# Kernel optimization log

Hardware: AMD Instinct MI355X
Metric: run time of the kernel (lower is better)

## Reference

```python
import jax, jax.numpy as jnp
import numpy as np
from jax.scipy.special import logsumexp

B, L, DIN, H, NL, E = 32, 1024, 2048, 1024, 21, 768
LN_EPS = 1e-5

def setup_inputs() -> dict:
    key = jax.random.key(0)
    ks = jax.random.split(key, 8)
    return {
        "seq_feats": jax.random.normal(ks[0], (B, L, DIN), jnp.float32),
        "labels": jax.random.randint(ks[1], (B, L), 0, NL),
        "attention_mask": jnp.ones((B, L), jnp.bool_),
        "W_tok": jax.random.normal(ks[2], (DIN, H), jnp.float32) * 0.02,
        "ln_gamma": jnp.ones((H,), jnp.float32),
        "ln_beta": jnp.zeros((H,), jnp.float32),
        "label_table": jax.random.normal(ks[3], (NL, E), jnp.float32) * 0.02,
        "W_lab": jax.random.normal(ks[4], (E, H), jnp.float32) * 0.02,
        "temperature": jnp.float32(10.0),
        "start_trans": jax.random.uniform(ks[5], (NL,), jnp.float32, -0.1, 0.1),
        "end_trans": jax.random.uniform(ks[6], (NL,), jnp.float32, -0.1, 0.1),
        "trans": jax.random.uniform(ks[7], (NL, NL), jnp.float32, -0.1, 0.1),
    }

def _crf_nll(logits, labels, mask, start_trans, end_trans, trans):
    # torchcrf CRF(batch_first=True), reduction='mean': loss = -mean_b llh_b
    mf = mask.astype(logits.dtype)  # (B,L)
    # --- numerator: score of the gold path ---
    emit = jnp.take_along_axis(logits, labels[..., None], axis=-1)[..., 0]  # (B,L)
    score = start_trans[labels[:, 0]] + emit[:, 0]
    score = score + (emit[:, 1:] * mf[:, 1:]).sum(-1)
    score = score + (trans[labels[:, :-1], labels[:, 1:]] * mf[:, 1:]).sum(-1)
    last_idx = mask.sum(-1).astype(jnp.int32) - 1  # (B,)
    last_tag = jnp.take_along_axis(labels, last_idx[:, None], axis=1)[:, 0]
    score = score + end_trans[last_tag]
    # --- denominator: log partition via forward algorithm (lax.scan over time) ---
    alpha0 = start_trans[None, :] + logits[:, 0]  # (B,NL)
    def step(alpha, xs):
        emit_t, m_t = xs  # (B,NL), (B,)
        new = logsumexp(alpha[:, :, None] + trans[None, :, :] + emit_t[:, None, :], axis=1)
        return jnp.where(m_t[:, None], new, alpha), None
    xs = (jnp.moveaxis(logits[:, 1:], 1, 0), jnp.moveaxis(mask[:, 1:], 1, 0))
    alpha, _ = jax.lax.scan(step, alpha0, xs)
    logZ = logsumexp(alpha + end_trans[None, :], axis=-1)  # (B,)
    return -(score - logZ).mean()

def reference(seq_feats, labels, attention_mask, W_tok, ln_gamma, ln_beta,
              label_table, W_lab, temperature, start_trans, end_trans, trans):
    # token_proj: Linear(no bias) -> LayerNorm -> GELU (exact) -> Dropout(eval=no-op)
    h = seq_feats @ W_tok  # (B,L,H)
    mu = h.mean(-1, keepdims=True)
    var = h.var(-1, keepdims=True)
    h = (h - mu) / jnp.sqrt(var + LN_EPS) * ln_gamma + ln_beta
    token_h = jax.nn.gelu(h, approximate=False)
    label_h = label_table @ W_lab  # (NL,H)
    logits = jnp.einsum('blh,nh->bln', token_h, label_h) * temperature
    loss = _crf_nll(logits, labels, attention_mask, start_trans, end_trans, trans)
    return logits, loss
```

## Files before the change

kernel.cpp:

```cpp
#include <hip/hip_runtime.h>
#include <math.h>

typedef __attribute__((ext_vector_type(8))) short bf16x8;
typedef __attribute__((ext_vector_type(4))) float f32x4;
typedef unsigned short u16;

#define Bsz 32
#define Lsz 1024
#define DIN 2048
#define Hsz 1024
#define NLB 21
#define CCH 64
#define TCH 16

__device__ __forceinline__ float b2f(u16 u) {
  union { unsigned int i; float f; } v; v.i = ((unsigned int)u) << 16; return v.f;
}
__device__ __forceinline__ u16 f2b(float f) {
  union { float f; unsigned int i; } v; v.f = f;
  unsigned int r = v.i + 0x7fffu + ((v.i >> 16) & 1u);
  return (u16)(r >> 16);
}

__global__ void k_convA(const float* __restrict__ in, u16* __restrict__ out, int n4) {
  int idx = blockIdx.x * blockDim.x + threadIdx.x;
  int stride = gridDim.x * blockDim.x;
  const float4* in4 = (const float4*)in;
  ushort4* out4 = (ushort4*)out;
  for (int i = idx; i < n4; i += stride) {
    float4 v = in4[i];
    ushort4 o;
    o.x = f2b(v.x); o.y = f2b(v.y); o.z = f2b(v.z); o.w = f2b(v.w);
    out4[i] = o;
  }
}

__global__ void k_convWT(const float* __restrict__ W, u16* __restrict__ Wt) {
  __shared__ float tile[64][65];
  const int ntile = blockIdx.x & 15;
  const int ktile = blockIdx.x >> 4;
  const int n0 = ntile * 64, k0 = ktile * 64;
  const int tid = threadIdx.x;
#pragma unroll
  for (int i = 0; i < 16; ++i) {
    int lin = i * 256 + tid;
    int r = lin >> 6, c = lin & 63;
    tile[r][c] = W[(size_t)(k0 + r) * Hsz + n0 + c];
  }
  __syncthreads();
#pragma unroll
  for (int i = 0; i < 16; ++i) {
    int lin = i * 256 + tid;
    int r = lin >> 6, c = lin & 63;
    Wt[(size_t)(n0 + r) * DIN + k0 + c] = f2b(tile[c][r]);
  }
}

__global__ void k_trW(const float* __restrict__ WL, float* __restrict__ WLt) {
  __shared__ float tile[64][65];
  const int nt = blockIdx.x & 15;
  const int et = blockIdx.x >> 4;
  const int n0 = nt * 64, e0 = et * 64;
  const int tid = threadIdx.x;
#pragma unroll
  for (int i = 0; i < 16; ++i) {
    int lin = i * 256 + tid;
    int r = lin >> 6, c = lin & 63;
    tile[r][c] = WL[(size_t)(e0 + r) * Hsz + n0 + c];
  }
  __syncthreads();
#pragma unroll
  for (int i = 0; i < 16; ++i) {
    int lin = i * 256 + tid;
    int r = lin >> 6, c = lin & 63;
    WLt[(size_t)(n0 + r) * 768 + e0 + c] = tile[c][r];
  }
}

__global__ __launch_bounds__(256) void k_labelh(const float* __restrict__ LT, const float* __restrict__ WLt,
                                                u16* __restrict__ LH) {
  const int tid = threadIdx.x;
  const int lane = tid & 63;
  const int wave = tid >> 6;
  const int wid = blockIdx.x * 4 + wave;
  const int row = wid >> 10;
  const int col = wid & 1023;
  const float4* a4 = (const float4*)(LT + (size_t)row * 768);
  const float4* b4 = (const float4*)(WLt + (size_t)col * 768);
  float p = 0.f;
#pragma unroll
  for (int it = 0; it < 3; ++it) {
    float4 a = a4[it * 64 + lane];
    float4 b = b4[it * 64 + lane];
    p += a.x * b.x + a.y * b.y + a.z * b.z + a.w * b.w;
  }
#pragma unroll
  for (int o = 32; o; o >>= 1) p += __shfl_xor(p, o);
  if (lane == 0) LH[(size_t)row * Hsz + col] = f2b(p);
}

__global__ __launch_bounds__(256) void k_gemm(const u16* __restrict__ A, const u16* __restrict__ Bt,
                                              u16* __restrict__ H) {
  __shared__ u16 sA[128 * 64];
  __shared__ u16 sB[128 * 64];
  const int tid = threadIdx.x;
  const int lane = tid & 63;
  const int wave = tid >> 6;
  const int m0 = (blockIdx.x >> 3) * 128;
  const int n0 = (blockIdx.x & 7) * 128;
  const int wm = (wave >> 1) * 64;
  const int wn = (wave & 1) * 64;

  f32x4 acc[4][4];
#pragma unroll
  for (int i = 0; i < 4; ++i)
#pragma unroll
    for (int j = 0; j < 4; ++j) acc[i][j] = (f32x4){0.f, 0.f, 0.f, 0.f};

  for (int k0 = 0; k0 < DIN; k0 += 64) {
#pragma unroll
    for (int q = 0; q < 4; ++q) {
      int idx = q * 256 + tid;
      int row = idx >> 3;
      int cl = (idx & 7) ^ (row & 7);
      const u16* ga = A + (size_t)(m0 + row) * DIN + k0 + cl * 8;
      __builtin_amdgcn_global_load_lds((const __attribute__((address_space(1))) void*)ga,
                                       (__attribute__((address_space(3))) void*)&sA[idx * 8], 16, 0, 0);
      const u16* gb = Bt + (size_t)(n0 + row) * DIN + k0 + cl * 8;
      __builtin_amdgcn_global_load_lds((const __attribute__((address_space(1))) void*)gb,
                                       (__attribute__((address_space(3))) void*)&sB[idx * 8], 16, 0, 0);
    }
    __syncthreads();
#pragma unroll
    for (int ks = 0; ks < 2; ++ks) {
      bf16x8 af[4], bfr[4];
      const int quad = lane >> 4;
      const int ck = ks * 4 + quad;
#pragma unroll
      for (int t = 0; t < 4; ++t) {
        int m = wm + t * 16 + (lane & 15);
        af[t] = *(const bf16x8*)&sA[m * 64 + ((ck ^ (m & 7)) * 8)];
        int n = wn + t * 16 + (lane & 15);
        bfr[t] = *(const bf16x8*)&sB[n * 64 + ((ck ^ (n & 7)) * 8)];
      }
#pragma unroll
      for (int i = 0; i < 4; ++i)
#pragma unroll
        for (int j = 0; j < 4; ++j)
          acc[i][j] = __builtin_amdgcn_mfma_f32_16x16x32_bf16(af[i], bfr[j], acc[i][j], 0, 0, 0);
    }
    __syncthreads();
  }
#pragma unroll
  for (int i = 0; i < 4; ++i) {
#pragma unroll
    for (int j = 0; j < 4; ++j) {
      int col = n0 + wn + j * 16 + (lane & 15);
      int r0 = m0 + wm + i * 16 + ((lane >> 4) << 2);
#pragma unroll
      for (int r = 0; r < 4; ++r) H[(size_t)(r0 + r) * Hsz + col] = f2b(acc[i][j][r]);
    }
  }
}

__global__ __launch_bounds__(256) void k_head(const u16* __restrict__ Hb, const u16* __restrict__ LH,
                                              const float* __restrict__ gamma, const float* __restrict__ beta,
                                              const float* __restrict__ tempp, float* __restrict__ logits) {
  __shared__ u16 sLH[32 * Hsz];
  const int tid = threadIdx.x;
  const int lane = tid & 63;
  const int wave = tid >> 6;
  for (int id = tid; id < 32 * 64; id += 256) {
    int n = id >> 6, c = id & 63;
    uint4 v = (uint4){0u, 0u, 0u, 0u};
    if (n < NLB) v = *(const uint4*)(LH + (size_t)n * Hsz + c * 8);
    *(uint4*)&sLH[((n << 6) | ((c & 56) | ((c ^ n) & 7))) * 8] = v;
  }
  const float T = tempp[0];
  __syncthreads();

  const int m = lane & 15;
  const int q = lane >> 4;
  const int tok = blockIdx.x * 64 + wave * 16 + m;
  const u16* arow = Hb + (size_t)tok * Hsz;

  float s = 0.f, s2 = 0.f;
  for (int kc = 0; kc < 32; ++kc) {
    bf16x8 v = *(const bf16x8*)(arow + kc * 32 + q * 8);
#pragma unroll
    for (int j = 0; j < 8; ++j) {
      float x = b2f(((const u16*)&v)[j]);
      s += x; s2 += x * x;
    }
  }
  s += __shfl_xor(s, 16);  s += __shfl_xor(s, 32);
  s2 += __shfl_xor(s2, 16); s2 += __shfl_xor(s2, 32);
  const float mu = s * (1.0f / 1024.0f);
  const float rstd = rsqrtf(s2 * (1.0f / 1024.0f) - mu * mu + 1e-5f);

  f32x4 acc0 = (f32x4){0.f, 0.f, 0.f, 0.f};
  f32x4 acc1 = (f32x4){0.f, 0.f, 0.f, 0.f};
  const int nr = lane & 15;
  for (int kc = 0; kc < 32; ++kc) {
    const int k = kc * 32 + q * 8;
    bf16x8 v = *(const bf16x8*)(arow + k);
    float4 g0 = *(const float4*)(gamma + k);
    float4 g1 = *(const float4*)(gamma + k + 4);
    float4 e0 = *(const float4*)(beta + k);
    float4 e1 = *(const float4*)(beta + k + 4);
    float gs[8] = {g0.x, g0.y, g0.z, g0.w, g1.x, g1.y, g1.z, g1.w};
    float bs[8] = {e0.x, e0.y, e0.z, e0.w, e1.x, e1.y, e1.z, e1.w};
    bf16x8 a;
#pragma unroll
    for (int j = 0; j < 8; ++j) {
      float x = b2f(((const u16*)&v)[j]);
      float y = (x - mu) * rstd * gs[j] + bs[j];
      float gl = 0.5f * y * (1.0f + erff(y * 0.70710678118654752f));
      ((u16*)&a)[j] = f2b(gl);
    }
    const int c = kc * 4 + q;
    const int cs = (c & 56) | ((c ^ nr) & 7);
    bf16x8 b0 = *(const bf16x8*)&sLH[((nr << 6) | cs) * 8];
    bf16x8 b1 = *(const bf16x8*)&sLH[(((16 + nr) << 6) | cs) * 8];
    acc0 = __builtin_amdgcn_mfma_f32_16x16x32_bf16(a, b0, acc0, 0, 0, 0);
    acc1 = __builtin_amdgcn_mfma_f32_16x16x32_bf16(a, b1, acc1, 0, 0, 0);
  }
  const int rbase = blockIdx.x * 64 + wave * 16 + q * 4;
#pragma unroll
  for (int r = 0; r < 4; ++r) {
    logits[(size_t)(rbase + r) * NLB + nr] = acc0[r] * T;
    if (nr < 5) logits[(size_t)(rbase + r) * NLB + 16 + nr] = acc1[r] * T;
  }
}

__global__ __launch_bounds__(256) void k_crf1(const float* __restrict__ logits,
                                              const float* __restrict__ trans,
                                              float* __restrict__ Mexp, float* __restrict__ Rlog,
                                              float* __restrict__ loss) {
  __shared__ float sEt[NLB * 24];
  const int tid = threadIdx.x;
  for (int idx = tid; idx < NLB * NLB; idx += 256) {
    int jj = idx / NLB, kk = idx % NLB;
    sEt[jj * 24 + kk] = __expf(trans[kk * NLB + jj]);
  }
  if (blockIdx.x == 0 && tid == 0) *loss = 0.f;
  __syncthreads();

  const int lane = tid & 63;
  const int wave = tid >> 6;
  const int pg = lane >= 42 ? 2 : (lane >= 21 ? 1 : 0);
  const int i0 = lane - pg * 21;
  const bool maskv0 = (lane < 63);
  const int i = i0 > 20 ? 20 : i0;
  const int prob_raw = (blockIdx.x * 4 + wave) * 3 + pg;
  const bool maskv = maskv0 && (prob_raw < Bsz * CCH);
  const int prob = prob_raw < Bsz * CCH ? prob_raw : Bsz * CCH - 1;
  const int b = prob >> 6;
  const int c = prob & 63;
  const int t0 = 1 + c * TCH;
  const float* lg = logits + (size_t)b * Lsz * NLB;

  float P[NLB], rlog = 0.f;
#pragma unroll
  for (int j = 0; j < NLB; ++j)
    P[j] = sEt[j * 24 + i] * __expf(lg[t0 * NLB + j]);
  {
    float m = P[0];
#pragma unroll
    for (int j = 1; j < NLB; ++j) m = fmaxf(m, P[j]);
    rlog = __logf(m);
    float r = 1.0f / m;
#pragma unroll
    for (int j = 0; j < NLB; ++j) P[j] *= r;
  }

  for (int tt = 1; tt < TCH; ++tt) {
    const int t = t0 + tt;
    if (t >= Lsz) break;
    float q[NLB];
#pragma unroll
    for (int j = 0; j < NLB; ++j) {
      const float* e = &sEt[j * 24];
      float4 e0 = *(const float4*)(e);
      float4 e1 = *(const float4*)(e + 4);
      float4 e2 = *(const float4*)(e + 8);
      float4 e3 = *(const float4*)(e + 12);
      float4 e4 = *(const float4*)(e + 16);
      float e5 = e[20];
      float s = P[0] * e0.x + P[1] * e0.y + P[2] * e0.z + P[3] * e0.w
              + P[4] * e1.x + P[5] * e1.y + P[6] * e1.z + P[7] * e1.w
              + P[8] * e2.x + P[9] * e2.y + P[10] * e2.z + P[11] * e2.w
              + P[12] * e3.x + P[13] * e3.y + P[14] * e3.z + P[15] * e3.w
              + P[16] * e4.x + P[17] * e4.y + P[18] * e4.z + P[19] * e4.w
              + P[20] * e5;
      q[j] = s * __expf(lg[t * NLB + j]);
    }
    float m = q[0];
#pragma unroll
    for (int j = 1; j < NLB; ++j) m = fmaxf(m, q[j]);
    rlog += __logf(m);
    float r = 1.0f / m;
#pragma unroll
    for (int j = 0; j < NLB; ++j) P[j] = q[j] * r;
  }

  if (maskv) {
    float* mo = Mexp + ((size_t)prob * NLB + i) * NLB;
#pragma unroll
    for (int j = 0; j < NLB; ++j) mo[j] = P[j];
    Rlog[(size_t)prob * NLB + i] = rlog;
  }
}

__global__ __launch_bounds__(64) void k_crf2(const float* __restrict__ logits, const int* __restrict__ labels,
                                             const float* __restrict__ startt, const float* __restrict__ endt,
                                             const float* __restrict__ trans,
                                             const float* __restrict__ Mexp, const float* __restrict__ Rlog,
                                             float* __restrict__ loss) {
  const int b = blockIdx.x;
  const int lane = threadIdx.x;
  const float* lg = logits + (size_t)b * Lsz * NLB;
  const int* lab = labels + (size_t)b * Lsz;

  float sc = 0.f;
  for (int t = lane; t < Lsz; t += 64) {
    int lt = lab[t];
    sc += lg[t * NLB + lt];
    if (t > 0) sc += trans[lab[t - 1] * NLB + lt];
  }
#pragma unroll
  for (int o = 32; o; o >>= 1) sc += __shfl_xor(sc, o);
  if (lane == 0) sc += startt[lab[0]] + endt[lab[Lsz - 1]];
  const float score = __shfl(sc, 0);

  const bool act = (lane < NLB);
  const int jc = act ? lane : NLB - 1;
  float a0 = act ? (startt[lane] + lg[lane]) : -INFINITY;
  float m = a0;
#pragma unroll
  for (int o = 32; o; o >>= 1) m = fmaxf(m, __shfl_xor(m, o));
  float p = act ? __expf(a0 - m) : 0.f;
  float macc = m;

  for (int c = 0; c < CCH; ++c) {
    const size_t prob = (size_t)b * CCH + c;
    float li = __logf(p) + Rlog[prob * NLB + jc];
    if (!act) li = -INFINITY;
    float S = li;
#pragma unroll
    for (int o = 32; o; o >>= 1) S = fmaxf(S, __shfl_xor(S, o));
    float w = __expf(li - S);
    const float* mc = Mexp + prob * (NLB * NLB) + jc;
    float q0 = 0.f, q1 = 0.f, q2 = 0.f;
#pragma unroll
    for (int ii = 0; ii < NLB; ii += 3) {
      q0 += __shfl(w, ii) * mc[ii * NLB];
      if (ii + 1 < NLB) q1 += __shfl(w, ii + 1) * mc[(ii + 1) * NLB];
      if (ii + 2 < NLB) q2 += __shfl(w, ii + 2) * mc[(ii + 2) * NLB];
    }
    float q = act ? (q0 + q1 + q2) : 0.f;
    float mx = q;
#pragma unroll
    for (int o = 32; o; o >>= 1) mx = fmaxf(mx, __shfl_xor(mx, o));
    p = q * (1.0f / mx);
    macc += S + __logf(mx);
  }

  float z = act ? p * __expf(endt[lane]) : 0.f;
#pragma unroll
  for (int o = 32; o; o >>= 1) z += __shfl_xor(z, o);
  if (lane == 0) {
    float logZ = macc + __logf(z);
    atomicAdd(loss, (logZ - score) * (1.0f / 32.0f));
  }
}

extern "C" void kernel_launch(void* const* d_in, const int* in_sizes, int n_in,
                              void* d_out, int out_size, void* d_ws, size_t ws_size,
                              hipStream_t stream) {
  const float* seq   = (const float*)d_in[0];
  const int*   labs  = (const int*)d_in[1];
  const float* Wtok  = (const float*)d_in[3];
  const float* gamma = (const float*)d_in[4];
  const float* beta  = (const float*)d_in[5];
  const float* LT    = (const float*)d_in[6];
  const float* WL    = (const float*)d_in[7];
  const float* temp  = (const float*)d_in[8];
  const float* st    = (const float*)d_in[9];
  const float* en    = (const float*)d_in[10];
  const float* tr    = (const float*)d_in[11];

  float* logits = (float*)d_out;
  float* loss   = logits + (size_t)Bsz * Lsz * NLB;

  char* ws = (char*)d_ws;
  u16* Abf   = (u16*)(ws);
  u16* Hbf   = (u16*)(ws + 134217728);
  float* WLt = (float*)(ws + 134217728);
  u16* Wt    = (u16*)(ws + 201326592);
  u16* LH    = (u16*)(ws + 205520896);
  float* Mexp = (float*)(ws);
  float* Rlog = (float*)(ws + 3612672);

  k_convA <<<dim3(4096), dim3(256), 0, stream>>>(seq, Abf, (Bsz * Lsz * DIN) / 4);
  k_convWT<<<dim3(512),  dim3(256), 0, stream>>>(Wtok, Wt);
  k_trW   <<<dim3(192),  dim3(256), 0, stream>>>(WL, WLt);
  k_labelh<<<dim3(5376), dim3(256), 0, stream>>>(LT, WLt, LH);
  k_gemm  <<<dim3(2048), dim3(256), 0, stream>>>(Abf, Wt, Hbf);
  k_head  <<<dim3(512),  dim3(256), 0, stream>>>(Hbf, LH, gamma, beta, temp, logits);
  k_crf1  <<<dim3(171),  dim3(256), 0, stream>>>(logits, tr, Mexp, Rlog, loss);
  k_crf2  <<<dim3(32),   dim3(64),  0, stream>>>(logits, labs, st, en, tr, Mexp, Rlog, loss);
}
```

Measured before the change: 730.3 us.

## Rewrite token GEMM as 256x256 double-buffered pipelined MFMA kernel

Replaces the 128x128 single-buffered bf16 GEMM with a 256x256 tile, 8-wave kernel. It uses double-buffered LDS and interleaves staged global-to-LDS loads with MFMA quarter-blocks, plus explicit vmcnt waits, barriers and setprio. Block indices are remapped so neighbouring blocks share A rows for better L2 reuse. The aim is to hide memory latency and raise arithmetic intensity in the dominant GEMM, at the cost of 128KB of LDS, high register pressure, and fragile hand-tuned wait counts.

```diff
diff --git a/kernel.cpp b/kernel.cpp
--- a/kernel.cpp
+++ b/kernel.cpp
@@ -99,66 +99,120 @@
   if (lane == 0) LH[(size_t)row * Hsz + col] = f2b(p);
 }
 
-__global__ __launch_bounds__(256) void k_gemm(const u16* __restrict__ A, const u16* __restrict__ Bt,
-                                              u16* __restrict__ H) {
-  __shared__ u16 sA[128 * 64];
-  __shared__ u16 sB[128 * 64];
+#define BAR() do { __builtin_amdgcn_sched_barrier(0); __builtin_amdgcn_s_barrier(); \
+                   __builtin_amdgcn_sched_barrier(0); } while (0)
+
+#define STAGE_A(bufi, h, kt2) do { \
+  _Pragma("unroll") \
+  for (int it_ = 0; it_ < 2; ++it_) { \
+    int row_ = it_ * 128 + (h) * 64 + r0; \
+    const u16* s_ = Ab + (size_t)row_ * DIN + (size_t)(kt2) * 64 + cl * 8; \
+    __builtin_amdgcn_global_load_lds((const __attribute__((address_space(1))) void*)s_, \
+        (__attribute__((address_space(3))) void*)&sA[bufi][row_ * 64 + (tid & 7) * 8], 16, 0, 0); \
+  } } while (0)
+
+#define STAGE_B(bufi, h, kt2) do { \
+  _Pragma("unroll") \
+  for (int it_ = 0; it_ < 2; ++it_) { \
+    int row_ = (it_ * 2 + (r0 >> 5)) * 64 + (h) * 32 + (r0 & 31); \
+    const u16* s_ = Bb + (size_t)row_ * DIN + (size_t)(kt2) * 64 + cl * 8; \
+    __builtin_amdgcn_global_load_lds((const __attribute__((address_space(1))) void*)s_, \
+        (__attribute__((address_space(3))) void*)&sB[bufi][row_ * 64 + (tid & 7) * 8], 16, 0, 0); \
+  } } while (0)
+
+#define LDA4(dst, sbuf, mh) do { \
+  _Pragma("unroll") for (int ks_ = 0; ks_ < 2; ++ks_) \
+  _Pragma("unroll") for (int mf_ = 0; mf_ < 4; ++mf_) { \
+    int rr_ = wm + (mh) * 64 + mf_ * 16 + (lane & 15); \
+    int ck_ = ks_ * 4 + (lane >> 4); \
+    dst[mf_][ks_] = *(const bf16x8*)&sA[sbuf][rr_ * 64 + ((ck_ ^ (rr_ & 7)) * 8)]; \
+  } } while (0)
+
+#define LDB2(dst, sbuf, nh) do { \
+  _Pragma("unroll") for (int ks_ = 0; ks_ < 2; ++ks_) \
+  _Pragma("unroll") for (int nf_ = 0; nf_ < 2; ++nf_) { \
+    int rr_ = wn + (nh) * 32 + nf_ * 16 + (lane & 15); \
+    int ck_ = ks_ * 4 + (lane >> 4); \
+    dst[nf_][ks_] = *(const bf16x8*)&sB[sbuf][rr_ * 64 + ((ck_ ^ (rr_ & 7)) * 8)]; \
+  } } while (0)
+
+#define MM(aarr, barr, mb, nb) do { \
+  __builtin_amdgcn_s_setprio(1); \
+  _Pragma("unroll") for (int ks_ = 0; ks_ < 2; ++ks_) \
+  _Pragma("unroll") for (int mf_ = 0; mf_ < 4; ++mf_) \
+  _Pragma("unroll") for (int nf_ = 0; nf_ < 2; ++nf_) \
+    acc[(mb) + mf_][(nb) + nf_] = __builtin_amdgcn_mfma_f32_16x16x32_bf16( \
+        aarr[mf_][ks_], barr[nf_][ks_], acc[(mb) + mf_][(nb) + nf_], 0, 0, 0); \
+  __builtin_amdgcn_s_setprio(0); \
+} while (0)
+
+__global__ __launch_bounds__(512, 2) void k_gemm(const u16* __restrict__ A, const u16* __restrict__ Bt,
+                                                 u16* __restrict__ H) {
+  __shared__ u16 sA[2][256 * 64];
+  __shared__ u16 sB[2][256 * 64];
   const int tid = threadIdx.x;
   const int lane = tid & 63;
   const int wave = tid >> 6;
-  const int m0 = (blockIdx.x >> 3) * 128;
-  const int n0 = (blockIdx.x & 7) * 128;
-  const int wm = (wave >> 1) * 64;
-  const int wn = (wave & 1) * 64;
-
-  f32x4 acc[4][4];
-#pragma unroll
-  for (int i = 0; i < 4; ++i)
+  const int bid = blockIdx.x;
+  const int lid = (bid & 7) * 64 + (bid >> 3);
+  const int m0 = (lid >> 2) * 256;
+  const int n0 = (lid & 3) * 256;
+  const int wm = (wave >> 2) * 128;
+  const int wn = (wave & 3) * 64;
+  const u16* Ab = A + (size_t)m0 * DIN;
+  const u16* Bb = Bt + (size_t)n0 * DIN;
+  const int r0 = tid >> 3;
+  const int cl = (tid & 7) ^ (r0 & 7);
+
+  f32x4 acc[8][4];
+#pragma unroll
+  for (int i = 0; i < 8; ++i)
 #pragma unroll
     for (int j = 0; j < 4; ++j) acc[i][j] = (f32x4){0.f, 0.f, 0.f, 0.f};
 
-  for (int k0 = 0; k0 < DIN; k0 += 64) {
-#pragma unroll
-    for (int q = 0; q < 4; ++q) {
-      int idx = q * 256 + tid;
-      int row = idx >> 3;
-      int cl = (idx & 7) ^ (row & 7);
-      const u16* ga = A + (size_t)(m0 + row) * DIN + k0 + cl * 8;
-      __builtin_amdgcn_global_load_lds((const __attribute__((address_space(1))) void*)ga,
-                                       (__attribute__((address_space(3))) void*)&sA[idx * 8], 16, 0, 0);
-      const u16* gb = Bt + (size_t)(n0 + row) * DIN + k0 + cl * 8;
-      __builtin_amdgcn_global_load_lds((const __attribute__((address_space(1))) void*)gb,
-                                       (__attribute__((address_space(3))) void*)&sB[idx * 8], 16, 0, 0);
-    }
-    __syncthreads();
-#pragma unroll
-    for (int ks = 0; ks < 2; ++ks) {
-      bf16x8 af[4], bfr[4];
-      const int quad = lane >> 4;
-      const int ck = ks * 4 + quad;
-#pragma unroll
-      for (int t = 0; t < 4; ++t) {
-        int m = wm + t * 16 + (lane & 15);
-        af[t] = *(const bf16x8*)&sA[m * 64 + ((ck ^ (m & 7)) * 8)];
-        int n = wn + t * 16 + (lane & 15);
-        bfr[t] = *(const bf16x8*)&sB[n * 64 + ((ck ^ (n & 7)) * 8)];
-      }
-#pragma unroll
-      for (int i = 0; i < 4; ++i)
-#pragma unroll
-        for (int j = 0; j < 4; ++j)
-          acc[i][j] = __builtin_amdgcn_mfma_f32_16x16x32_bf16(af[i], bfr[j], acc[i][j], 0, 0, 0);
-    }
-    __syncthreads();
-  }
-#pragma unroll
-  for (int i = 0; i < 4; ++i) {
-#pragma unroll
-    for (int j = 0; j < 4; ++j) {
-      int col = n0 + wn + j * 16 + (lane & 15);
-      int r0 = m0 + wm + i * 16 + ((lane >> 4) << 2);
-#pragma unroll
-      for (int r = 0; r < 4; ++r) H[(size_t)(r0 + r) * Hsz + col] = f2b(acc[i][j][r]);
+  STAGE_A(0, 0, 0); STAGE_B(0, 0, 0); STAGE_A(0, 1, 0); STAGE_B(0, 1, 0);
+  STAGE_A(1, 0, 1); STAGE_B(1, 0, 1); STAGE_A(1, 1, 1);
+  asm volatile("s_waitcnt vmcnt(6)" ::: "memory");
+  BAR();
+
+  bf16x8 a[4][2], b0[2][2], b1[2][2];
+  const int NT = DIN / 64;
+  for (int t = 0; t < NT; ++t) {
+    const int cur = t & 1, nxt = cur ^ 1;
+    const bool p1 = (t + 1 < NT);
+    const bool p2 = (t + 2 < NT);
+    LDA4(a, cur, 0);
+    LDB2(b0, cur, 0);
+    if (p1) STAGE_B(nxt, 1, t + 1);
+    BAR();
+    MM(a, b0, 0, 0);
+    BAR();
+    LDB2(b1, cur, 1);
+    if (p2) STAGE_A(cur, 0, t + 2);
+    BAR();
+    MM(a, b1, 0, 2);
+    BAR();
+    LDA4(a, cur, 1);
+    if (p2) STAGE_B(cur, 0, t + 2);
+    BAR();
+    MM(a, b1, 4, 2);
+    BAR();
+    if (p2) STAGE_A(cur, 1, t + 2);
+    if (t < NT - 2)       { asm volatile("s_waitcnt vmcnt(6)" ::: "memory"); }
+    else if (t == NT - 2) { asm volatile("s_waitcnt vmcnt(0)" ::: "memory"); }
+    BAR();
+    MM(a, b0, 4, 0);
+    BAR();
+  }
+
+#pragma unroll
+  for (int mf = 0; mf < 8; ++mf) {
+#pragma unroll
+    for (int nf = 0; nf < 4; ++nf) {
+      int col = n0 + wn + nf * 16 + (lane & 15);
+      int er = m0 + wm + mf * 16 + ((lane >> 4) << 2);
+#pragma unroll
+      for (int r = 0; r < 4; ++r) H[(size_t)(er + r) * Hsz + col] = f2b(acc[mf][nf][r]);
     }
   }
 }
@@ -406,7 +460,7 @@
   k_convWT<<<dim3(512),  dim3(256), 0, stream>>>(Wtok, Wt);
   k_trW   <<<dim3(192),  dim3(256), 0, stream>>>(WL, WLt);
   k_labelh<<<dim3(5376), dim3(256), 0, stream>>>(LT, WLt, LH);
-  k_gemm  <<<dim3(2048), dim3(256), 0, stream>>>(Abf, Wt, Hbf);
+  k_gemm  <<<dim3(512),  dim3(512), 0, stream>>>(Abf, Wt, Hbf);
   k_head  <<<dim3(512),  dim3(256), 0, stream>>>(Hbf, LH, gamma, beta, temp, logits);
   k_crf1  <<<dim3(171),  dim3(256), 0, stream>>>(logits, tr, Mexp, Rlog, loss);
   k_crf2  <<<dim3(32),   dim3(64),  0, stream>>>(logits, labs, st, en, tr, Mexp, Rlog, loss);
```

Result: no change. 733.4 us (+0.4%).
